# Kernel tuning notes

Measured on AMD Instinct MI355X. Metric: run time of the kernel, lower is better.

Reference implementation:

```python
import jax, jax.numpy as jnp
import numpy as np

B, S, H, D = 2, 2048, 16, 64
HID = H * D


def setup_inputs() -> dict:
    key = jax.random.key(0)
    ks = jax.random.split(key, 9)
    s = 1.0 / np.sqrt(HID)
    return {
        "x": jax.random.normal(ks[0], (B, S, HID), dtype=jnp.float32),
        "Wq": jax.random.normal(ks[1], (HID, HID), dtype=jnp.float32) * s,
        "bq": jax.random.normal(ks[2], (HID,), dtype=jnp.float32) * s,
        "Wk": jax.random.normal(ks[3], (HID, HID), dtype=jnp.float32) * s,
        "bk": jax.random.normal(ks[4], (HID,), dtype=jnp.float32) * s,
        "Wv": jax.random.normal(ks[5], (HID, HID), dtype=jnp.float32) * s,
        "bv": jax.random.normal(ks[6], (HID,), dtype=jnp.float32) * s,
        "Wp": jax.random.normal(ks[7], (HID, HID), dtype=jnp.float32) * s,
        "bp": jax.random.normal(ks[8], (HID,), dtype=jnp.float32) * s,
    }


def reference(x, Wq, bq, Wk, bk, Wv, bv, Wp, bp):
    b, s, hid = x.shape
    d = hid // H
    # linear projections (torch Linear: x @ W.T + b), split heads -> [b, h, s, d]
    def heads(y):
        return y.reshape(b, s, H, d).transpose(0, 2, 1, 3)
    q = heads(x @ Wq.T + bq)
    k = heads(x @ Wk.T + bk)
    v = heads(x @ Wv.T + bv)
    scale = 1.0 / np.sqrt(d).astype(np.float32)
    att = jnp.einsum("bhqd,bhkd->bhqk", q, k) * scale
    causal = jnp.tril(jnp.ones((s, s), dtype=bool))  # [s, s]
    att = jnp.where(causal[None, None], att, -jnp.inf)
    att = jax.nn.softmax(att, axis=-1)
    y = jnp.einsum("bhqk,bhkd->bhqd", att, v)
    y = y.transpose(0, 2, 1, 3).reshape(b, s, hid)
    return y @ Wp.T + bp
```

## Files before the change

kernel.cpp:

```cpp
#include <hip/hip_runtime.h>


typedef unsigned short u16;
typedef float f32x4 __attribute__((ext_vector_type(4)));
typedef __bf16 bf16x8 __attribute__((ext_vector_type(8)));
typedef unsigned short u16x4 __attribute__((ext_vector_type(4)));
typedef unsigned short u16x8 __attribute__((ext_vector_type(8)));

constexpr int Bn = 2, SEQ = 2048, NH = 16, HD = 64, HID = 1024;
constexpr size_t NX = (size_t)Bn * SEQ * HID;
constexpr size_t NW = (size_t)HID * HID;

__device__ __forceinline__ u16 f2bf(float f) {
  unsigned u = __float_as_uint(f);
  u += 0x7fff + ((u >> 16) & 1);
  return (u16)(u >> 16);
}

__device__ __forceinline__ f32x4 mfma16(bf16x8 a, bf16x8 b, f32x4 c) {
  return __builtin_amdgcn_mfma_f32_16x16x32_bf16(a, b, c, 0, 0, 0);
}

__device__ __forceinline__ void gload16(const u16* g, u16* l) {
  __builtin_amdgcn_global_load_lds(
      (const __attribute__((address_space(1))) unsigned int*)(const void*)g,
      (__attribute__((address_space(3))) unsigned int*)(void*)l, 16, 0, 0);
}

__global__ void cvt_all(const float* __restrict__ x,
                        const float* __restrict__ Wq, const float* __restrict__ Wk,
                        const float* __restrict__ Wv, const float* __restrict__ Wp,
                        u16* __restrict__ xb, u16* __restrict__ wqb, u16* __restrict__ wkb,
                        u16* __restrict__ wvb, u16* __restrict__ wpb) {
  size_t i = ((size_t)blockIdx.x * blockDim.x + threadIdx.x) * 4;
  const float* s; u16* d; size_t off;
  if (i < NX) { s = x; d = xb; off = i; }
  else {
    size_t k = i - NX;
    int id = (int)(k >> 20);
    off = k & (NW - 1);
    s = (id == 0) ? Wq : (id == 1) ? Wk : (id == 2) ? Wv : Wp;
    d = (id == 0) ? wqb : (id == 1) ? wkb : (id == 2) ? wvb : wpb;
  }
  float4 v = *reinterpret_cast<const float4*>(s + off);
  u16x4 o = {f2bf(v.x), f2bf(v.y), f2bf(v.z), f2bf(v.w)};
  *reinterpret_cast<u16x4*>(d + off) = o;
}

__global__ __launch_bounds__(256) void qkv_gemm(
    const u16* __restrict__ A,
    const u16* __restrict__ W0, const u16* __restrict__ W1, const u16* __restrict__ W2,
    const float* __restrict__ b0, const float* __restrict__ b1, const float* __restrict__ b2,
    u16* __restrict__ out0, u16* __restrict__ out1, u16* __restrict__ out2)
{
  constexpr int K = HID;
  __shared__ u16 smem[16384];
  const int tid = threadIdx.x;
  const int lane = tid & 63, w = tid >> 6;
  const int wr = w >> 1, wc = w & 1;
  const int l15 = lane & 15, g = lane >> 4;
  const int m0 = blockIdx.y * 128;
  const int n0g = blockIdx.x * 128;
  const int id = n0g >> 10;
  const int n0 = n0g & (HID - 1);
  const u16* Bm = (id == 0) ? W0 : (id == 1) ? W1 : W2;
  const float* bias = (id == 0) ? b0 : (id == 1) ? b1 : b2;

  auto stage = [&](int buf, int kt) {
#pragma unroll
    for (int i = 0; i < 2; i++) {
      int chunk = tid + 256 * i;
      int r = chunk >> 2, c = (chunk & 3) << 3;
      gload16(&A[(size_t)(m0 + r) * K + kt + c], &smem[buf * 4096 + chunk * 8]);
      gload16(&Bm[(size_t)(n0 + r) * K + kt + c], &smem[8192 + buf * 4096 + chunk * 8]);
    }
  };

  f32x4 acc[4][4] = {};
  stage(0, 0);

  for (int ki = 0; ki < 32; ki++) {
    const int buf = ki & 1;
    __syncthreads();
    if (ki + 1 < 32) stage(buf ^ 1, (ki + 1) * 32);
    const u16* As = &smem[buf * 4096];
    const u16* Bs = &smem[8192 + buf * 4096];
    bf16x8 af[4], bfr[4];
#pragma unroll
    for (int mi = 0; mi < 4; mi++)
      af[mi] = *reinterpret_cast<const bf16x8*>(&As[(wr * 64 + mi * 16 + l15) * 32 + g * 8]);
#pragma unroll
    for (int ni = 0; ni < 4; ni++)
      bfr[ni] = *reinterpret_cast<const bf16x8*>(&Bs[(wc * 64 + ni * 16 + l15) * 32 + g * 8]);
#pragma unroll
    for (int mi = 0; mi < 4; mi++)
#pragma unroll
      for (int ni = 0; ni < 4; ni++)
        acc[mi][ni] = mfma16(af[mi], bfr[ni], acc[mi][ni]);
  }

  float bv[4];
#pragma unroll
  for (int ni = 0; ni < 4; ni++) bv[ni] = bias[n0 + wc * 64 + ni * 16 + l15];

  if (id == 2) {
    __syncthreads();
#pragma unroll
    for (int mi = 0; mi < 4; mi++)
#pragma unroll
      for (int ni = 0; ni < 4; ni++) {
        u16x4 pk;
#pragma unroll
        for (int r = 0; r < 4; r++) pk[r] = f2bf(acc[mi][ni][r] + bv[ni]);
        int d_loc = wc * 64 + ni * 16 + l15;
        int sq_base = wr * 64 + mi * 16 + g * 4;
        *reinterpret_cast<u16x4*>(
            &smem[d_loc * 128 + (sq_base ^ ((d_loc & 7) << 4))]) = pk;
      }
    __syncthreads();
    const int bb = m0 >> 11;
    const int sq0 = m0 & (SEQ - 1);
#pragma unroll
    for (int i = 0; i < 8; i++) {
      int chunk = tid + 256 * i;
      int d_loc = chunk >> 4;
      int sqc = (chunk & 15) << 3;
      u16x8 val = *reinterpret_cast<const u16x8*>(
          &smem[d_loc * 128 + (sqc ^ ((d_loc & 7) << 4))]);
      int gn = n0 + d_loc;
      int hh = gn >> 6, dd = gn & 63;
      *reinterpret_cast<u16x8*>(
          &out2[((size_t)(bb * NH + hh) * HD + dd) * SEQ + sq0 + sqc]) = val;
    }
  } else {
    u16* out = (id == 0) ? out0 : out1;
#pragma unroll
    for (int mi = 0; mi < 4; mi++)
#pragma unroll
      for (int ni = 0; ni < 4; ni++)
#pragma unroll
        for (int r = 0; r < 4; r++) {
          int gm = m0 + wr * 64 + mi * 16 + g * 4 + r;
          int gn = n0 + wc * 64 + ni * 16 + l15;
          int bb = gm >> 11, sq = gm & (SEQ - 1);
          int hh = gn >> 6, d = gn & 63;
          out[((size_t)(bb * NH + hh) * SEQ + sq) * HD + d] = f2bf(acc[mi][ni][r] + bv[ni]);
        }
  }
}

__global__ __launch_bounds__(256) void gemm_out(
    const u16* __restrict__ A, const u16* __restrict__ Bm,
    const float* __restrict__ bias, float* __restrict__ out)
{
  constexpr int K = HID, N = HID;
  __shared__ u16 As[2][64 * 32];
  __shared__ u16 Bs[2][128 * 32];
  const int tid = threadIdx.x;
  const int lane = tid & 63, w = tid >> 6;
  const int l15 = lane & 15, g = lane >> 4;
  const int m0 = blockIdx.y * 64, n0 = blockIdx.x * 128;

  auto stage = [&](int buf, int kt) {
    {
      int r = tid >> 2, c = (tid & 3) << 3;
      gload16(&A[(size_t)(m0 + r) * K + kt + c], &As[buf][tid * 8]);
    }
#pragma unroll
    for (int i = 0; i < 2; i++) {
      int chunk = tid + 256 * i;
      int r = chunk >> 2, c = (chunk & 3) << 3;
      gload16(&Bm[(size_t)(n0 + r) * K + kt + c], &Bs[buf][chunk * 8]);
    }
  };

  f32x4 acc[4][2] = {};
  stage(0, 0);

  for (int ki = 0; ki < 32; ki++) {
    const int buf = ki & 1;
    __syncthreads();
    if (ki + 1 < 32) stage(buf ^ 1, (ki + 1) * 32);
    bf16x8 af[4], bfr[2];
#pragma unroll
    for (int mi = 0; mi < 4; mi++)
      af[mi] = *reinterpret_cast<const bf16x8*>(&As[buf][(mi * 16 + l15) * 32 + g * 8]);
#pragma unroll
    for (int ni = 0; ni < 2; ni++)
      bfr[ni] = *reinterpret_cast<const bf16x8*>(&Bs[buf][(w * 32 + ni * 16 + l15) * 32 + g * 8]);
#pragma unroll
    for (int mi = 0; mi < 4; mi++)
#pragma unroll
      for (int ni = 0; ni < 2; ni++)
        acc[mi][ni] = mfma16(af[mi], bfr[ni], acc[mi][ni]);
  }

  float bv[2];
#pragma unroll
  for (int ni = 0; ni < 2; ni++) bv[ni] = bias[n0 + w * 32 + ni * 16 + l15];

#pragma unroll
  for (int mi = 0; mi < 4; mi++)
#pragma unroll
    for (int ni = 0; ni < 2; ni++)
#pragma unroll
      for (int r = 0; r < 4; r++) {
        int gm = m0 + mi * 16 + g * 4 + r;
        int gn = n0 + w * 32 + ni * 16 + l15;
        out[(size_t)gm * N + gn] = acc[mi][ni][r] + bv[ni];
      }
}

__global__ __launch_bounds__(256, 4) void attn_kernel(
    const u16* __restrict__ Q, const u16* __restrict__ Kt,
    const u16* __restrict__ Vt, u16* __restrict__ Y)
{
  __shared__ u16 smK[2][4096];
  __shared__ u16 smV[2][4096];
  const int tid = threadIdx.x;
  const int lane = tid & 63, w = tid >> 6;
  const int l15 = lane & 15, g = lane >> 4;
  const int bid = blockIdx.x;
  const int q = bid >> 8;
  const int rr = bid & 255;
  const int xcd = rr & 7;
  const int cu = (rr >> 3) & 31;
  const int bh = xcd * 4 + (cu & 3);
  const int s = cu >> 2;
  int tile;
  if (q == 0) tile = 24 + s;
  else if (q == 1) tile = 23 - s;
  else if (q == 2) tile = 8 + s;
  else tile = 7 - s;
  const int b = bh >> 4, h = bh & 15;
  const int xs = l15 & 7;

  const int nt = tile + 1;
  const int q0 = tile * 64 + w * 16;
  const int qg = q0 + l15;

  const size_t bhs = (size_t)bh;
  const u16* Qp = Q + bhs * SEQ * HD;
  const u16* Kp = Kt + bhs * SEQ * HD;
  const u16* Vp = Vt + bhs * HD * SEQ;

  int srow[2], sslot[2];
#pragma unroll
  for (int it = 0; it < 2; it++) {
    int idx = it * 256 + tid;
    srow[it] = idx >> 3;
    sslot[it] = (idx & 7) ^ (srow[it] & 7);
  }
  auto stage = [&](int buf, int kt) {
#pragma unroll
    for (int it = 0; it < 2; it++) {
      int idx = it * 256 + tid;
      gload16(Kp + (size_t)(kt + srow[it]) * HD + sslot[it] * 8, &smK[buf][idx * 8]);
      gload16(Vp + (size_t)srow[it] * SEQ + kt + sslot[it] * 8, &smV[buf][idx * 8]);
    }
  };

  const float QSC = 0.125f * 1.44269504088896f;
  const float NEG = -__builtin_inff();

  bf16x8 tq0 = *reinterpret_cast<const bf16x8*>(Qp + (size_t)qg * HD + g * 8);
  bf16x8 tq1 = *reinterpret_cast<const bf16x8*>(Qp + (size_t)qg * HD + 32 + g * 8);
  stage(0, 0);
  bf16x8 qf[2];
#pragma unroll
  for (int jj = 0; jj < 8; jj++) {
    qf[0][jj] = (__bf16)((float)tq0[jj] * QSC);
    qf[1][jj] = (__bf16)((float)tq1[jj] * QSC);
  }

  float m_run = NEG;
  float l_lane = 0.0f;
  f32x4 o[4] = {};

  auto iter_body = [&](int t, bool MASKED) __attribute__((always_inline)) {
    const int kt = t * 64;
    const int buf = t & 1;
    __syncthreads();
    if (t + 1 < nt) stage(buf ^ 1, kt + 64);
    const u16* K_ = smK[buf];
    const u16* V_ = smV[buf];

    f32x4 sa[4];
#pragma unroll
    for (int sub = 0; sub < 4; sub++) {
      int row = sub * 16 + l15;
      bf16x8 k0 = *reinterpret_cast<const bf16x8*>(&K_[row * 64 + ((0 + g) ^ xs) * 8]);
      bf16x8 k1 = *reinterpret_cast<const bf16x8*>(&K_[row * 64 + ((4 + g) ^ xs) * 8]);
      f32x4 a = {0.f, 0.f, 0.f, 0.f};
      a = mfma16(k0, qf[0], a);
      a = mfma16(k1, qf[1], a);
      sa[sub] = a;
    }

    float p[16];
    if (MASKED) {
#pragma unroll
      for (int sub = 0; sub < 4; sub++)
#pragma unroll
        for (int r = 0; r < 4; r++) {
          int key = kt + sub * 16 + g * 4 + r;
          p[sub * 4 + r] = (key <= qg) ? sa[sub][r] : NEG;
        }
    } else {
#pragma unroll
      for (int sub = 0; sub < 4; sub++)
#pragma unroll
        for (int r = 0; r < 4; r++) p[sub * 4 + r] = sa[sub][r];
    }

    float a0 = fmaxf(fmaxf(p[0], p[1]), p[2]);
    float a1 = fmaxf(fmaxf(p[3], p[4]), p[5]);
    float a2 = fmaxf(fmaxf(p[6], p[7]), p[8]);
    float a3 = fmaxf(fmaxf(p[9], p[10]), p[11]);
    float a4 = fmaxf(fmaxf(p[12], p[13]), p[14]);
    float b0 = fmaxf(fmaxf(a0, a1), p[15]);
    float tloc = fmaxf(fmaxf(b0, a2), fmaxf(a3, a4));

    if (__any(tloc > m_run + 11.0f)) {
      float tmax = tloc;
      tmax = fmaxf(tmax, __shfl_xor(tmax, 16));
      tmax = fmaxf(tmax, __shfl_xor(tmax, 32));
      float mnew = fmaxf(m_run, tmax);
      float fs = __builtin_amdgcn_exp2f(m_run - mnew);
      l_lane *= fs;
#pragma unroll
      for (int db = 0; db < 4; db++) o[db] *= fs;
      m_run = mnew;
    }

    float pe[16];
    float s4[4] = {0.f, 0.f, 0.f, 0.f};
#pragma unroll
    for (int i = 0; i < 16; i++) {
      pe[i] = __builtin_amdgcn_exp2f(p[i] - m_run);
      s4[i & 3] += pe[i];
    }

#pragma unroll
    for (int half = 0; half < 2; half++) {
      bf16x8 pb;
#pragma unroll
      for (int jj = 0; jj < 8; jj++) pb[jj] = (__bf16)pe[8 * half + jj];
      const int s0 = ((4 * half + (g >> 1)) ^ xs) * 8 + 4 * (g & 1);
      const int s1 = ((4 * half + 2 + (g >> 1)) ^ xs) * 8 + 4 * (g & 1);
#pragma unroll
      for (int db = 0; db < 4; db++) {
        int vbase = (db * 16 + l15) * 64;
        u16x4 v0 = *reinterpret_cast<const u16x4*>(&V_[vbase + s0]);
        u16x4 v1 = *reinterpret_cast<const u16x4*>(&V_[vbase + s1]);
        u16x8 vau;
#pragma unroll
        for (int jj = 0; jj < 4; jj++) { vau[jj] = v0[jj]; vau[jj + 4] = v1[jj]; }
        bf16x8 va = __builtin_bit_cast(bf16x8, vau);
        o[db] = mfma16(va, pb, o[db]);
      }
    }

    l_lane += (s4[0] + s4[1]) + (s4[2] + s4[3]);
  };

  for (int t = 0; t < nt - 1; t++) iter_body(t, false);
  iter_body(nt - 1, true);

  float l_tot = l_lane;
  l_tot += __shfl_xor(l_tot, 16);
  l_tot += __shfl_xor(l_tot, 32);
  float rl = 1.0f / l_tot;
#pragma unroll
  for (int db = 0; db < 4; db++) {
    u16x4 yo;
#pragma unroll
    for (int r = 0; r < 4; r++) yo[r] = f2bf(o[db][r] * rl);
    *reinterpret_cast<u16x4*>(
        Y + ((size_t)(b * SEQ) + qg) * HID + h * HD + db * 16 + g * 4) = yo;
  }
}

extern "C" void kernel_launch(void* const* d_in, const int* in_sizes, int n_in,
                              void* d_out, int out_size, void* d_ws, size_t ws_size,
                              hipStream_t stream) {
  const float* x  = (const float*)d_in[0];
  const float* Wq = (const float*)d_in[1];
  const float* bq = (const float*)d_in[2];
  const float* Wk = (const float*)d_in[3];
  const float* bk = (const float*)d_in[4];
  const float* Wv = (const float*)d_in[5];
  const float* bv = (const float*)d_in[6];
  const float* Wp = (const float*)d_in[7];
  const float* bp = (const float*)d_in[8];

  u16* ws = (u16*)d_ws;
  u16* xb  = ws; ws += NX;
  u16* wqb = ws; ws += NW;
  u16* wkb = ws; ws += NW;
  u16* wvb = ws; ws += NW;
  u16* wpb = ws; ws += NW;
  u16* Qb  = ws; ws += NX;
  u16* Kb  = ws; ws += NX;
  u16* Vtb = ws; ws += NX;
  u16* Yb  = ws; ws += NX;

  const unsigned cvtBlocks = (unsigned)((NX + 4 * NW) / 4 / 256);
  cvt_all<<<cvtBlocks, 256, 0, stream>>>(x, Wq, Wk, Wv, Wp, xb, wqb, wkb, wvb, wpb);

  qkv_gemm<<<dim3(24, 32), 256, 0, stream>>>(xb, wqb, wkb, wvb, bq, bk, bv, Qb, Kb, Vtb);

  attn_kernel<<<dim3(1024), 256, 0, stream>>>(Qb, Kb, Vtb, Yb);

  gemm_out<<<dim3(8, 64), 256, 0, stream>>>(Yb, wpb, bp, (float*)d_out);
}
```

Before: 114.3 us.

## Split long causal attention tiles into KV partitions with a combine kernel

Query tiles 16-31 are split into two KV-range partitions, so the attention grid grows to 1536 blocks. Table-driven scheduling balances iteration counts across blocks. Split partials (unnormalized O in bf16 plus per-row max and sum) go to reused workspace buffers (xb, wqb), and a new combine kernel merges them with log-sum-exp weighting. The aim is to cut load imbalance and tail effects of the causal triangle, at the cost of an extra launch, partial-output traffic and bf16 rounding of the partials.

```diff
diff --git a/kernel.cpp b/kernel.cpp
--- a/kernel.cpp
+++ b/kernel.cpp
@@ -11,10 +11,31 @@
 constexpr size_t NX = (size_t)Bn * SEQ * HID;
 constexpr size_t NW = (size_t)HID * HID;
 
+__device__ __constant__ unsigned char PT_TILE[48] = {
+  31,31,30,15, 30,29,29,28,14, 28,27,27,26,13, 26,25,25,24,12,
+  24,23,23,22,11, 22,21,21,20,10, 20,19,19,18,9, 18,17,17,16,8,
+  16,7, 6,5,4,3,2,1,0};
+__device__ __constant__ unsigned char PT_PART[48] = {
+  1,2,1,0, 2,1,2,1,0, 2,1,2,1,0, 2,1,2,1,0,
+  2,1,2,1,0, 2,1,2,1,0, 2,1,2,1,0, 2,1,2,1,0,
+  2,0, 0,0,0,0,0,0,0};
+__device__ __constant__ unsigned char PT_START[48] = {
+  0,16,0,0, 16,0,15,0,0, 15,0,14,0,0, 14,0,13,0,0,
+  13,0,12,0,0, 12,0,11,0,0, 11,0,10,0,0, 10,0,9,0,0,
+  9,0, 0,0,0,0,0,0,0};
+__device__ __constant__ unsigned char PT_NIT[48] = {
+  16,16,16,16, 15,15,15,15,15, 14,14,14,14,14, 13,13,13,13,13,
+  12,12,12,12,12, 11,11,11,11,11, 10,10,10,10,10, 9,9,9,9,9,
+  8,8, 7,6,5,4,3,2,1};
+
 __device__ __forceinline__ u16 f2bf(float f) {
   unsigned u = __float_as_uint(f);
   u += 0x7fff + ((u >> 16) & 1);
   return (u16)(u >> 16);
+}
+
+__device__ __forceinline__ float bf2f(u16 u) {
+  return __uint_as_float(((unsigned)u) << 16);
 }
 
 __device__ __forceinline__ f32x4 mfma16(bf16x8 a, bf16x8 b, f32x4 c) {
@@ -213,7 +234,8 @@
 
 __global__ __launch_bounds__(256, 4) void attn_kernel(
     const u16* __restrict__ Q, const u16* __restrict__ Kt,
-    const u16* __restrict__ Vt, u16* __restrict__ Y)
+    const u16* __restrict__ Vt, u16* __restrict__ Y,
+    u16* __restrict__ OP, float2* __restrict__ MLP)
 {
   __shared__ u16 smK[2][4096];
   __shared__ u16 smV[2][4096];
@@ -221,21 +243,17 @@
   const int lane = tid & 63, w = tid >> 6;
   const int l15 = lane & 15, g = lane >> 4;
   const int bid = blockIdx.x;
-  const int q = bid >> 8;
-  const int rr = bid & 255;
-  const int xcd = rr & 7;
-  const int cu = (rr >> 3) & 31;
-  const int bh = xcd * 4 + (cu & 3);
-  const int s = cu >> 2;
-  int tile;
-  if (q == 0) tile = 24 + s;
-  else if (q == 1) tile = 23 - s;
-  else if (q == 2) tile = 8 + s;
-  else tile = 7 - s;
+  const int xcd = bid & 7;
+  const int r_ = bid >> 3;
+  const int bh = xcd * 4 + (r_ & 3);
+  const int piece = r_ >> 2;
+  const int tile = PT_TILE[piece];
+  const int part = PT_PART[piece];
+  const int it0 = PT_START[piece];
+  const int nit = PT_NIT[piece];
   const int b = bh >> 4, h = bh & 15;
   const int xs = l15 & 7;
 
-  const int nt = tile + 1;
   const int q0 = tile * 64 + w * 16;
   const int qg = q0 + l15;
 
@@ -265,7 +283,7 @@
 
   bf16x8 tq0 = *reinterpret_cast<const bf16x8*>(Qp + (size_t)qg * HD + g * 8);
   bf16x8 tq1 = *reinterpret_cast<const bf16x8*>(Qp + (size_t)qg * HD + 32 + g * 8);
-  stage(0, 0);
+  stage(0, it0 * 64);
   bf16x8 qf[2];
 #pragma unroll
   for (int jj = 0; jj < 8; jj++) {
@@ -277,11 +295,11 @@
   float l_lane = 0.0f;
   f32x4 o[4] = {};
 
-  auto iter_body = [&](int t, bool MASKED) __attribute__((always_inline)) {
-    const int kt = t * 64;
-    const int buf = t & 1;
+  auto iter_body = [&](int i, bool MASKED) __attribute__((always_inline)) {
+    const int kt = (it0 + i) * 64;
+    const int buf = i & 1;
     __syncthreads();
-    if (t + 1 < nt) stage(buf ^ 1, kt + 64);
+    if (i + 1 < nit) stage(buf ^ 1, kt + 64);
     const u16* K_ = smK[buf];
     const u16* V_ = smV[buf];
 
@@ -336,9 +354,9 @@
     float pe[16];
     float s4[4] = {0.f, 0.f, 0.f, 0.f};
 #pragma unroll
-    for (int i = 0; i < 16; i++) {
-      pe[i] = __builtin_amdgcn_exp2f(p[i] - m_run);
-      s4[i & 3] += pe[i];
+    for (int i2 = 0; i2 < 16; i2++) {
+      pe[i2] = __builtin_amdgcn_exp2f(p[i2] - m_run);
+      s4[i2 & 3] += pe[i2];
     }
 
 #pragma unroll
@@ -364,21 +382,81 @@
     l_lane += (s4[0] + s4[1]) + (s4[2] + s4[3]);
   };
 
-  for (int t = 0; t < nt - 1; t++) iter_body(t, false);
-  iter_body(nt - 1, true);
+  if (part == 1) {
+    for (int i = 0; i < nit; i++) iter_body(i, false);
+  } else {
+    for (int i = 0; i < nit - 1; i++) iter_body(i, false);
+    iter_body(nit - 1, true);
+  }
 
   float l_tot = l_lane;
   l_tot += __shfl_xor(l_tot, 16);
   l_tot += __shfl_xor(l_tot, 32);
-  float rl = 1.0f / l_tot;
-#pragma unroll
-  for (int db = 0; db < 4; db++) {
-    u16x4 yo;
-#pragma unroll
-    for (int r = 0; r < 4; r++) yo[r] = f2bf(o[db][r] * rl);
-    *reinterpret_cast<u16x4*>(
-        Y + ((size_t)(b * SEQ) + qg) * HID + h * HD + db * 16 + g * 4) = yo;
-  }
+
+  if (part == 0) {
+    float rl = 1.0f / l_tot;
+#pragma unroll
+    for (int db = 0; db < 4; db++) {
+      u16x4 yo;
+#pragma unroll
+      for (int r = 0; r < 4; r++) yo[r] = f2bf(o[db][r] * rl);
+      *reinterpret_cast<u16x4*>(
+          Y + ((size_t)(b * SEQ) + qg) * HID + h * HD + db * 16 + g * 4) = yo;
+    }
+  } else {
+    const int slot = (bh * 16 + (tile - 16)) * 2 + (part - 1);
+    u16* op = OP + (size_t)slot * 4096 + (w * 16 + l15) * 64;
+#pragma unroll
+    for (int db = 0; db < 4; db++) {
+      u16x4 po;
+#pragma unroll
+      for (int r = 0; r < 4; r++) po[r] = f2bf(o[db][r]);
+      *reinterpret_cast<u16x4*>(op + db * 16 + g * 4) = po;
+    }
+    if (g == 0) {
+      float2 ml; ml.x = m_run; ml.y = l_tot;
+      MLP[slot * 64 + w * 16 + l15] = ml;
+    }
+  }
+}
+
+__global__ __launch_bounds__(256) void attn_combine(
+    const u16* __restrict__ OP, const float2* __restrict__ MLP, u16* __restrict__ Y)
+{
+  const int bid = blockIdx.x;
+  const int xcd = bid & 7;
+  const int r_ = bid >> 3;
+  const int bh = xcd * 4 + (r_ & 3);
+  const int t16 = r_ >> 2;
+  const int tile = 16 + t16;
+  const int b = bh >> 4, h = bh & 15;
+  const int slotA = (bh * 16 + t16) * 2, slotB = slotA + 1;
+
+  const int t = threadIdx.x;
+  const int q = t >> 2, dc = (t & 3) << 4;
+
+  float2 mlA = MLP[slotA * 64 + q];
+  float2 mlB = MLP[slotB * 64 + q];
+  float m = fmaxf(mlA.x, mlB.x);
+  float wA = __builtin_amdgcn_exp2f(mlA.x - m);
+  float wB = __builtin_amdgcn_exp2f(mlB.x - m);
+  float rl = 1.0f / (mlA.y * wA + mlB.y * wB);
+
+  const u16* pa = OP + (size_t)slotA * 4096 + q * 64 + dc;
+  const u16* pb = OP + (size_t)slotB * 4096 + q * 64 + dc;
+  u16x8 a0 = *reinterpret_cast<const u16x8*>(pa);
+  u16x8 a1 = *reinterpret_cast<const u16x8*>(pa + 8);
+  u16x8 b0 = *reinterpret_cast<const u16x8*>(pb);
+  u16x8 b1 = *reinterpret_cast<const u16x8*>(pb + 8);
+  u16x8 y0, y1;
+#pragma unroll
+  for (int j = 0; j < 8; j++) {
+    y0[j] = f2bf((bf2f(a0[j]) * wA + bf2f(b0[j]) * wB) * rl);
+    y1[j] = f2bf((bf2f(a1[j]) * wA + bf2f(b1[j]) * wB) * rl);
+  }
+  u16* yp = Y + ((size_t)(b * SEQ) + tile * 64 + q) * HID + h * HD + dc;
+  *reinterpret_cast<u16x8*>(yp) = y0;
+  *reinterpret_cast<u16x8*>(yp + 8) = y1;
 }
 
 extern "C" void kernel_launch(void* const* d_in, const int* in_sizes, int n_in,
@@ -405,12 +483,17 @@
   u16* Vtb = ws; ws += NX;
   u16* Yb  = ws; ws += NX;
 
+  u16*    OP  = xb;
+  float2* MLP = (float2*)wqb;
+
   const unsigned cvtBlocks = (unsigned)((NX + 4 * NW) / 4 / 256);
   cvt_all<<<cvtBlocks, 256, 0, stream>>>(x, Wq, Wk, Wv, Wp, xb, wqb, wkb, wvb, wpb);
 
   qkv_gemm<<<dim3(24, 32), 256, 0, stream>>>(xb, wqb, wkb, wvb, bq, bk, bv, Qb, Kb, Vtb);
 
-  attn_kernel<<<dim3(1024), 256, 0, stream>>>(Qb, Kb, Vtb, Yb);
+  attn_kernel<<<dim3(1536), 256, 0, stream>>>(Qb, Kb, Vtb, Yb, OP, MLP);
+
+  attn_combine<<<dim3(512), 256, 0, stream>>>(OP, MLP, Yb);
 
   gemm_out<<<dim3(8, 64), 256, 0, stream>>>(Yb, wpb, bp, (float*)d_out);
 }
```

Measured after the change: 112.1 us. No clear change (-1.9%).
